# Performance work log

Hardware: AMD Instinct MI355X
Metric: run time of the kernel (lower is better)

Reference implementation:

```python
import jax, jax.numpy as jnp
import numpy as np

BETA = 0.9
THR = 1.0
ALPHA = 2.0  # snntorch surrogate.atan default

@jax.custom_vjp
def atan_spike(x):
    return (x > 0).astype(x.dtype)

def _atan_fwd(x):
    return atan_spike(x), x

def _atan_bwd(x, g):
    # snntorch ATan surrogate: alpha/2 / (1 + (pi/2 * alpha * x)^2)
    return (g * (ALPHA / 2.0) / (1.0 + (jnp.pi / 2.0 * ALPHA * x) ** 2),)

atan_spike.defvjp(_atan_fwd, _atan_bwd)

def setup_inputs() -> dict:
    key = jax.random.key(0)
    k = jax.random.split(key, 5)
    B, T, C, H, W = 128, 25, 3, 64, 64
    F, HID, O = C * H * W, 2048, 2
    bound1 = 1.0 / np.sqrt(F)
    boundo = 1.0 / np.sqrt(HID)
    return {
        "x": jax.random.normal(k[0], (B, T, C, H, W), jnp.float32),
        "W1": jax.random.uniform(k[1], (HID, F), jnp.float32, -bound1, bound1),
        "b1": jax.random.uniform(k[2], (HID,), jnp.float32, -bound1, bound1),
        "Wo": jax.random.uniform(k[3], (O, HID), jnp.float32, -boundo, boundo),
        "bo": jax.random.uniform(k[4], (O,), jnp.float32, -boundo, boundo),
    }

def reference(x, W1, b1, Wo, bo):
    B, T = x.shape[0], x.shape[1]
    HID, O = W1.shape[0], Wo.shape[0]
    xf = x.reshape(B, T, -1).transpose(1, 0, 2)  # [T, B, F]
    # fc1 for all timesteps at once (input is fixed per step)
    h_all = jnp.einsum('tbf,hf->tbh', xf, W1) + b1  # [T, B, HID]

    def step(carry, h):
        mem1, memo = carry
        # snntorch Leaky (reset_mechanism='subtract'): reset from previous mem
        r1 = atan_spike(mem1 - THR)
        mem1 = BETA * mem1 + h - r1 * THR
        s1 = atan_spike(mem1 - THR)
        o = s1 @ Wo.T + bo
        ro = atan_spike(memo - THR)
        memo = BETA * memo + o - ro * THR
        so = atan_spike(memo - THR)
        return (mem1, memo), so

    init = (jnp.zeros((B, HID), x.dtype), jnp.zeros((B, O), x.dtype))
    (_, _), spk_rec = jax.lax.scan(step, init, h_all)
    # train=False path: sum of output spikes over time
    return spk_rec.sum(axis=0)  # [B, O]
```

## Files before the change

kernel.cpp:

```cpp
#include <hip/hip_runtime.h>


#define T_STEPS 25
#define B_SZ    128
#define F_SZ    12288
#define HID_SZ  2048
#define KT      384
#define M_PAD   3328
#define UPB     156
#define PART_STRIDE ((size_t)M_PAD * HID_SZ)

typedef __attribute__((ext_vector_type(8))) _Float16 f16x8;
typedef __attribute__((ext_vector_type(4))) float f32x4;
typedef __attribute__((ext_vector_type(16))) float f32x16;

__device__ __forceinline__ void g2l16(const void* g, void* l) {
  __builtin_amdgcn_global_load_lds(
      (const __attribute__((address_space(1))) void*)g,
      (__attribute__((address_space(3))) void*)l, 16, 0, 0);
}

__device__ __forceinline__ void split8(f32x4 v0, f32x4 v1, f16x8& hi, f16x8& lo) {
#pragma unroll
  for (int j = 0; j < 4; ++j) {
    _Float16 h = (_Float16)v0[j];
    hi[j] = h;
    lo[j] = (_Float16)(v0[j] - (float)h);
    _Float16 h2 = (_Float16)v1[j];
    hi[4 + j] = h2;
    lo[4 + j] = (_Float16)(v1[j] - (float)h2);
  }
}

__global__ __launch_bounds__(256) void conv_w_kernel(
    const float* __restrict__ W1, char* __restrict__ B2) {
  const int total = 8 * KT * 256 * 4;
  for (int i = blockIdx.x * 256 + threadIdx.x; i < total; i += gridDim.x * 256) {
    const int s = i & 3;
    const int r = (i >> 2) & 255;
    const int rest = i >> 10;
    const int ks = rest % KT;
    const int nt = rest / KT;
    const float* src = W1 + ((size_t)(nt * 256 + r)) * F_SZ + ks * 32 + s * 8;
    float4 v0 = *(const float4*)src;
    float4 v1 = *(const float4*)(src + 4);
    float vf[8] = {v0.x, v0.y, v0.z, v0.w, v1.x, v1.y, v1.z, v1.w};
    f16x8 hi, lo;
#pragma unroll
    for (int j = 0; j < 8; ++j) {
      float vs = vf[j] * 128.0f;
      _Float16 h = (_Float16)vs;
      hi[j] = h;
      lo[j] = (_Float16)(vs - (float)h);
    }
    char* chunk = B2 + (size_t)rest * 32768;
    *(f16x8*)(chunk + s * 4096 + r * 16) = hi;
    *(f16x8*)(chunk + (s + 4) * 4096 + r * 16) = lo;
  }
}

__global__ __launch_bounds__(512, 1) void gemm_persist_kernel(
    const float* __restrict__ x, const char* __restrict__ B2,
    float* __restrict__ parts) {
  __shared__ __align__(16) char lds[131072];
  const int tid = threadIdx.x;
  const int l = tid & 63;
  const int w = tid >> 6;
  const int wm = w >> 2;
  const int wn = w & 3;
  const int lhalf = l >> 5;

  const int swz = ((blockIdx.x & 7) << 5) + (blockIdx.x >> 3);

  const int arow = (wm * 128 + (l & 31)) * 16;
  const int brow = (wn * 64 + (l & 31)) * 16;

  int u = swz * UPB;
  const int u1 = u + UPB;

  while (u < u1) {
    const int mnt = u / 384;
    const int kt0 = u - mnt * 384;
    const int rem_t = 384 - kt0, rem_u = u1 - u;
    const int seg = rem_t < rem_u ? rem_t : rem_u;
    const int ktN = kt0 + seg;
    const int nt = mnt / 13;
    const int mt = mnt - nt * 13;

    int m = mt * 256 + (tid & 255);
    if (m > 3199) m = 3199;
    const char* aRow = (const char*)(x +
        ((size_t)((m & 127) * T_STEPS + (m >> 7))) * F_SZ) + ((tid >> 8) << 4);
    const char* bBase = B2 + (size_t)nt * KT * 32768 + tid * 16;

#define STAGE(ktx)                                                        \
    do {                                                                  \
      char* d_ = (char*)lds + ((ktx) & 1) * 65536 + tid * 16;             \
      const char* as_ = aRow + (ktx) * 128;                               \
      const char* bs_ = bBase + (size_t)(ktx) * 32768;                    \
      g2l16(as_, d_);              g2l16(as_ + 32, d_ + 8192);            \
      g2l16(as_ + 64, d_ + 16384); g2l16(as_ + 96, d_ + 24576);           \
      g2l16(bs_, d_ + 32768);          g2l16(bs_ + 8192, d_ + 40960);     \
      g2l16(bs_ + 16384, d_ + 49152);  g2l16(bs_ + 24576, d_ + 57344);    \
    } while (0)

    f32x16 acc[4][2];
#pragma unroll
    for (int i = 0; i < 4; ++i)
#pragma unroll
      for (int j = 0; j < 2; ++j)
#pragma unroll
        for (int r = 0; r < 16; ++r) acc[i][j][r] = 0.f;

    STAGE(kt0);

    for (int kt = kt0; kt < ktN; ++kt) {
      __syncthreads();
      if (kt + 1 < ktN) STAGE(kt + 1);

      const char* la = (const char*)lds + (kt & 1) * 65536;
      const char* lb = la + 32768;

#pragma unroll
      for (int ks = 0; ks < 2; ++ks) {
        const int g = ks * 2 + lhalf;
        const int aBase = g * 8192 + arow;
        f16x8 ah[4], al[4];
#pragma unroll
        for (int mf = 0; mf < 4; ++mf) {
          f32x4 v0 = *(const f32x4*)(la + aBase + mf * 512);
          f32x4 v1 = *(const f32x4*)(la + aBase + 4096 + mf * 512);
          split8(v0, v1, ah[mf], al[mf]);
        }
#pragma unroll
        for (int nf = 0; nf < 2; ++nf) {
          f16x8 bh = *(const f16x8*)(lb + g * 4096 + brow + nf * 512);
          f16x8 bl = *(const f16x8*)(lb + 16384 + g * 4096 + brow + nf * 512);
          __builtin_amdgcn_s_setprio(1);
#pragma unroll
          for (int mf = 0; mf < 4; ++mf) {
            acc[mf][nf] = __builtin_amdgcn_mfma_f32_32x32x16_f16(ah[mf], bh, acc[mf][nf], 0, 0, 0);
            acc[mf][nf] = __builtin_amdgcn_mfma_f32_32x32x16_f16(ah[mf], bl, acc[mf][nf], 0, 0, 0);
            acc[mf][nf] = __builtin_amdgcn_mfma_f32_32x32x16_f16(al[mf], bh, acc[mf][nf], 0, 0, 0);
          }
          __builtin_amdgcn_s_setprio(0);
        }
      }
    }

    const int slot = swz - (mnt * 384) / UPB;
    float* dst = parts + (size_t)slot * PART_STRIDE;
    const int row0 = mt * 256 + wm * 128 + (lhalf << 2);
    const int col0 = nt * 256 + wn * 64 + (l & 31);
#pragma unroll
    for (int nf = 0; nf < 2; ++nf)
#pragma unroll
      for (int mf = 0; mf < 4; ++mf)
#pragma unroll
        for (int r = 0; r < 16; ++r) {
          const int row = row0 + mf * 32 + (r & 3) + ((r >> 2) << 3);
          dst[(size_t)row * HID_SZ + col0 + nf * 32] = acc[mf][nf][r];
        }
    u += seg;
    __syncthreads();
#undef STAGE
  }
}

__global__ __launch_bounds__(256) void gemm_h_kernel(
    const float* __restrict__ x, const float* __restrict__ W1,
    const float* __restrict__ b1, float* __restrict__ h_all) {
  __shared__ float As[16][128];
  __shared__ float Bs[16][128];
  const int tid = threadIdx.x;
  const int tx = tid & 15;
  const int ty = tid >> 4;
  const int m0 = blockIdx.x * 128;
  const int n0 = blockIdx.y * 128;
  const int lrow = tid >> 1;
  const int lcol = (tid & 1) * 8;
  const int gm = m0 + lrow;
  const int bb = gm & (B_SZ - 1);
  const int tt = gm >> 7;
  const float* aptr = x + ((size_t)bb * T_STEPS + tt) * F_SZ + lcol;
  const float* bptr = W1 + (size_t)(n0 + lrow) * F_SZ + lcol;
  float acc[8][8];
#pragma unroll
  for (int i = 0; i < 8; ++i)
#pragma unroll
    for (int j = 0; j < 8; ++j) acc[i][j] = 0.f;
  for (int k0 = 0; k0 < F_SZ; k0 += 16) {
    float4 av0 = *(const float4*)(aptr + k0);
    float4 av1 = *(const float4*)(aptr + k0 + 4);
    float4 bv0 = *(const float4*)(bptr + k0);
    float4 bv1 = *(const float4*)(bptr + k0 + 4);
    As[lcol + 0][lrow] = av0.x; As[lcol + 1][lrow] = av0.y;
    As[lcol + 2][lrow] = av0.z; As[lcol + 3][lrow] = av0.w;
    As[lcol + 4][lrow] = av1.x; As[lcol + 5][lrow] = av1.y;
    As[lcol + 6][lrow] = av1.z; As[lcol + 7][lrow] = av1.w;
    Bs[lcol + 0][lrow] = bv0.x; Bs[lcol + 1][lrow] = bv0.y;
    Bs[lcol + 2][lrow] = bv0.z; Bs[lcol + 3][lrow] = bv0.w;
    Bs[lcol + 4][lrow] = bv1.x; Bs[lcol + 5][lrow] = bv1.y;
    Bs[lcol + 6][lrow] = bv1.z; Bs[lcol + 7][lrow] = bv1.w;
    __syncthreads();
#pragma unroll
    for (int k = 0; k < 16; ++k) {
      float4 a0 = *(const float4*)&As[k][ty * 8];
      float4 a1 = *(const float4*)&As[k][ty * 8 + 4];
      float4 q0 = *(const float4*)&Bs[k][tx * 8];
      float4 q1 = *(const float4*)&Bs[k][tx * 8 + 4];
      float ar[8] = {a0.x, a0.y, a0.z, a0.w, a1.x, a1.y, a1.z, a1.w};
      float br[8] = {q0.x, q0.y, q0.z, q0.w, q1.x, q1.y, q1.z, q1.w};
#pragma unroll
      for (int i = 0; i < 8; ++i)
#pragma unroll
        for (int j = 0; j < 8; ++j)
          acc[i][j] = fmaf(ar[i], br[j], acc[i][j]);
    }
    __syncthreads();
  }
#pragma unroll
  for (int i = 0; i < 8; ++i) {
    const int gm2 = m0 + ty * 8 + i;
    float* orow = h_all + (size_t)gm2 * HID_SZ + n0 + tx * 8;
    const float* brow = b1 + n0 + tx * 8;
#pragma unroll
    for (int j = 0; j < 8; ++j) orow[j] = acc[i][j] + brow[j];
  }
}

__global__ __launch_bounds__(256) void lif_hidden_kernel(
    const float* __restrict__ parts, const float* __restrict__ b1,
    const float* __restrict__ Wo, float* __restrict__ oc, int mode) {
  const int b = blockIdx.x & 127;
  const int half = blockIdx.x >> 7;
  const int tid = threadIdx.x;
  const int h0 = half * 1024;
  float mem1[4], wo0[4], wo1[4], bv[4];
#pragma unroll
  for (int i = 0; i < 4; ++i) {
    const int hid = h0 + 256 * i + tid;
    mem1[i] = 0.f;
    wo0[i] = Wo[hid];
    wo1[i] = Wo[HID_SZ + hid];
    bv[i] = b1[hid];
  }
  __shared__ float partial[4][2];
  for (int t = 0; t < T_STEPS; ++t) {
    const int row = t * B_SZ + b;
    const size_t rowb = (size_t)row * HID_SZ;
    const int mt = row >> 8;
    float pr0 = 0.f, pr1 = 0.f;
#pragma unroll
    for (int i = 0; i < 4; ++i) {
      const int hid = h0 + 256 * i + tid;
      const size_t idx = rowb + hid;
      float h;
      if (mode == 2) {
        float s = parts[idx] + parts[idx + PART_STRIDE] +
                  parts[idx + 2 * PART_STRIDE];
        const int mnt = (hid >> 8) * 13 + mt;
        const int k0 = mnt * 384;
        if ((k0 + 383) / UPB - k0 / UPB + 1 == 4)
          s += parts[idx + 3 * PART_STRIDE];
        h = s * 0.0078125f + bv[i];
      } else {
        h = parts[idx];
      }
      float r1 = mem1[i] > 1.0f ? 1.0f : 0.0f;
      float m = 0.9f * mem1[i] + h - r1;
      mem1[i] = m;
      if (m > 1.0f) { pr0 += wo0[i]; pr1 += wo1[i]; }
    }
#pragma unroll
    for (int off = 32; off > 0; off >>= 1) {
      pr0 += __shfl_down(pr0, off);
      pr1 += __shfl_down(pr1, off);
    }
    if ((tid & 63) == 0) { partial[tid >> 6][0] = pr0; partial[tid >> 6][1] = pr1; }
    __syncthreads();
    if (tid == 0) {
      const size_t o = (((size_t)b * 2 + half) * T_STEPS + t) * 2;
      oc[o + 0] = partial[0][0] + partial[1][0] + partial[2][0] + partial[3][0];
      oc[o + 1] = partial[0][1] + partial[1][1] + partial[2][1] + partial[3][1];
    }
    __syncthreads();
  }
}

__global__ __launch_bounds__(128) void lif_out_kernel(
    const float* __restrict__ oc, const float* __restrict__ bo,
    float* __restrict__ out) {
  const int b = threadIdx.x;
  float memo0 = 0.f, memo1 = 0.f, a0 = 0.f, a1 = 0.f;
  const float bo0 = bo[0], bo1 = bo[1];
  for (int t = 0; t < T_STEPS; ++t) {
    const size_t i0 = (((size_t)b * 2 + 0) * T_STEPS + t) * 2;
    const size_t i1 = (((size_t)b * 2 + 1) * T_STEPS + t) * 2;
    float o0 = oc[i0] + oc[i1] + bo0;
    float o1 = oc[i0 + 1] + oc[i1 + 1] + bo1;
    float ro0 = memo0 > 1.0f ? 1.0f : 0.0f;
    float ro1 = memo1 > 1.0f ? 1.0f : 0.0f;
    memo0 = 0.9f * memo0 + o0 - ro0;
    memo1 = 0.9f * memo1 + o1 - ro1;
    a0 += memo0 > 1.0f ? 1.0f : 0.0f;
    a1 += memo1 > 1.0f ? 1.0f : 0.0f;
  }
  out[b * 2 + 0] = a0;
  out[b * 2 + 1] = a1;
}

extern "C" void kernel_launch(void* const* d_in, const int* in_sizes, int n_in,
                              void* d_out, int out_size, void* d_ws, size_t ws_size,
                              hipStream_t stream) {
  const float* x  = (const float*)d_in[0];
  const float* W1 = (const float*)d_in[1];
  const float* b1 = (const float*)d_in[2];
  const float* Wo = (const float*)d_in[3];
  const float* bo = (const float*)d_in[4];
  float* out = (float*)d_out;

  const size_t part_bytes = PART_STRIDE * 4;
  const size_t b2_bytes = (size_t)8 * KT * 32768;
  const size_t oc_bytes = (size_t)128 * 2 * T_STEPS * 2 * 4;
  char* ws = (char*)d_ws;
  float* parts = (float*)ws;

  if (ws_size >= 4 * part_bytes + b2_bytes + oc_bytes) {
    char* B2 = ws + 4 * part_bytes;
    float* oc = (float*)(B2 + b2_bytes);
    conv_w_kernel<<<2048, 256, 0, stream>>>(W1, B2);
    gemm_persist_kernel<<<256, 512, 0, stream>>>(x, B2, parts);
    lif_hidden_kernel<<<256, 256, 0, stream>>>(parts, b1, Wo, oc, 2);
    lif_out_kernel<<<1, 128, 0, stream>>>(oc, bo, out);
  } else {
    float* oc = (float*)(ws + part_bytes);
    dim3 grid(25, 16);
    gemm_h_kernel<<<grid, 256, 0, stream>>>(x, W1, b1, parts);
    lif_hidden_kernel<<<256, 256, 0, stream>>>(parts, b1, Wo, oc, 0);
    lif_out_kernel<<<1, 128, 0, stream>>>(oc, bo, out);
  }
}
```

Baseline: 672.1 us.

## Replace persistent stream-K GEMM with fixed split-K tiles and triple-buffered A staging

Replaces the persistent stream-K scheduler, in which 256 blocks walked a linear unit range, with a grid of 416 blocks. Each block owns one 256x256 tile and a fixed quarter of K (split-K by 4). The A operand now uses three LDS buffers staged two steps ahead, B uses two buffers, and explicit vmcnt waits with raw barriers replace __syncthreads. The LIF kernel sums all four partials unconditionally. This removes the segment bookkeeping and aims at deeper load/compute overlap, at the cost of more LDS per block and losing the balanced work distribution across CUs.

```diff
diff --git a/kernel.cpp b/kernel.cpp
--- a/kernel.cpp
+++ b/kernel.cpp
@@ -7,7 +7,6 @@
 #define HID_SZ  2048
 #define KT      384
 #define M_PAD   3328
-#define UPB     156
 #define PART_STRIDE ((size_t)M_PAD * HID_SZ)
 
 typedef __attribute__((ext_vector_type(8))) _Float16 f16x8;
@@ -59,10 +58,10 @@
   }
 }
 
-__global__ __launch_bounds__(512, 1) void gemm_persist_kernel(
+__global__ __launch_bounds__(512, 1) void gemm_tile_kernel(
     const float* __restrict__ x, const char* __restrict__ B2,
     float* __restrict__ parts) {
-  __shared__ __align__(16) char lds[131072];
+  __shared__ __align__(16) char lds[163840];
   const int tid = threadIdx.x;
   const int l = tid & 63;
   const int w = tid >> 6;
@@ -70,101 +69,113 @@
   const int wn = w & 3;
   const int lhalf = l >> 5;
 
-  const int swz = ((blockIdx.x & 7) << 5) + (blockIdx.x >> 3);
+  const int bid = blockIdx.x;
+  const int mt = bid >> 5;
+  const int nt = (bid >> 2) & 7;
+  const int ksp = bid & 3;
+  const int kt0 = ksp * 96;
+  const int ktN = kt0 + 96;
 
   const int arow = (wm * 128 + (l & 31)) * 16;
   const int brow = (wn * 64 + (l & 31)) * 16;
 
-  int u = swz * UPB;
-  const int u1 = u + UPB;
-
-  while (u < u1) {
-    const int mnt = u / 384;
-    const int kt0 = u - mnt * 384;
-    const int rem_t = 384 - kt0, rem_u = u1 - u;
-    const int seg = rem_t < rem_u ? rem_t : rem_u;
-    const int ktN = kt0 + seg;
-    const int nt = mnt / 13;
-    const int mt = mnt - nt * 13;
-
-    int m = mt * 256 + (tid & 255);
-    if (m > 3199) m = 3199;
-    const char* aRow = (const char*)(x +
-        ((size_t)((m & 127) * T_STEPS + (m >> 7))) * F_SZ) + ((tid >> 8) << 4);
-    const char* bBase = B2 + (size_t)nt * KT * 32768 + tid * 16;
-
-#define STAGE(ktx)                                                        \
-    do {                                                                  \
-      char* d_ = (char*)lds + ((ktx) & 1) * 65536 + tid * 16;             \
-      const char* as_ = aRow + (ktx) * 128;                               \
-      const char* bs_ = bBase + (size_t)(ktx) * 32768;                    \
-      g2l16(as_, d_);              g2l16(as_ + 32, d_ + 8192);            \
-      g2l16(as_ + 64, d_ + 16384); g2l16(as_ + 96, d_ + 24576);           \
-      g2l16(bs_, d_ + 32768);          g2l16(bs_ + 8192, d_ + 40960);     \
-      g2l16(bs_ + 16384, d_ + 49152);  g2l16(bs_ + 24576, d_ + 57344);    \
-    } while (0)
-
-    f32x16 acc[4][2];
-#pragma unroll
-    for (int i = 0; i < 4; ++i)
-#pragma unroll
-      for (int j = 0; j < 2; ++j)
-#pragma unroll
-        for (int r = 0; r < 16; ++r) acc[i][j][r] = 0.f;
-
-    STAGE(kt0);
-
-    for (int kt = kt0; kt < ktN; ++kt) {
-      __syncthreads();
-      if (kt + 1 < ktN) STAGE(kt + 1);
-
-      const char* la = (const char*)lds + (kt & 1) * 65536;
-      const char* lb = la + 32768;
-
-#pragma unroll
-      for (int ks = 0; ks < 2; ++ks) {
-        const int g = ks * 2 + lhalf;
-        const int aBase = g * 8192 + arow;
-        f16x8 ah[4], al[4];
+  int m = mt * 256 + (tid & 255);
+  if (m > 3199) m = 3199;
+  const char* aRow = (const char*)(x +
+      ((size_t)((m & 127) * T_STEPS + (m >> 7))) * F_SZ) + ((tid >> 8) << 4);
+  const char* bBase = B2 + (size_t)nt * KT * 32768 + tid * 16;
+
+#define STAGE_A(ktx, buf)                                                \
+  do {                                                                   \
+    char* d_ = (char*)lds + (buf) * 32768 + tid * 16;                    \
+    const char* s_ = aRow + (ktx) * 128;                                 \
+    g2l16(s_, d_);              g2l16(s_ + 32, d_ + 8192);               \
+    g2l16(s_ + 64, d_ + 16384); g2l16(s_ + 96, d_ + 24576);              \
+  } while (0)
+#define STAGE_B(ktx, buf)                                                \
+  do {                                                                   \
+    char* d_ = (char*)lds + 98304 + (buf) * 32768 + tid * 16;            \
+    const char* s_ = bBase + (size_t)(ktx) * 32768;                      \
+    g2l16(s_, d_);                  g2l16(s_ + 8192, d_ + 8192);         \
+    g2l16(s_ + 16384, d_ + 16384);  g2l16(s_ + 24576, d_ + 24576);       \
+  } while (0)
+
+  f32x16 acc[4][2];
+#pragma unroll
+  for (int i = 0; i < 4; ++i)
+#pragma unroll
+    for (int j = 0; j < 2; ++j)
+#pragma unroll
+      for (int r = 0; r < 16; ++r) acc[i][j][r] = 0.f;
+
+  STAGE_A(kt0, 0);
+  STAGE_B(kt0, 0);
+  STAGE_A(kt0 + 1, 1);
+
+  int ab = 0;
+  int ab2 = 2;
+  int bb = 0;
+
+  for (int kt = kt0; kt < ktN; ++kt) {
+    if (kt + 1 < ktN) {
+      asm volatile("s_waitcnt vmcnt(4)" ::: "memory");
+    } else {
+      asm volatile("s_waitcnt vmcnt(0)" ::: "memory");
+    }
+    __builtin_amdgcn_s_barrier();
+    __builtin_amdgcn_sched_barrier(0);
+
+    if (kt + 1 < ktN) STAGE_B(kt + 1, bb ^ 1);
+    if (kt + 2 < ktN) STAGE_A(kt + 2, ab2);
+
+    const char* la = (const char*)lds + ab * 32768;
+    const char* lb = (const char*)lds + 98304 + bb * 32768;
+
+#pragma unroll
+    for (int ks = 0; ks < 2; ++ks) {
+      const int g = ks * 2 + lhalf;
+      const int aBase = g * 8192 + arow;
+      f16x8 ah[4], al[4];
+#pragma unroll
+      for (int mf = 0; mf < 4; ++mf) {
+        f32x4 v0 = *(const f32x4*)(la + aBase + mf * 512);
+        f32x4 v1 = *(const f32x4*)(la + aBase + 4096 + mf * 512);
+        split8(v0, v1, ah[mf], al[mf]);
+      }
+#pragma unroll
+      for (int nf = 0; nf < 2; ++nf) {
+        f16x8 bh = *(const f16x8*)(lb + g * 4096 + brow + nf * 512);
+        f16x8 bl = *(const f16x8*)(lb + 16384 + g * 4096 + brow + nf * 512);
+        __builtin_amdgcn_s_setprio(1);
 #pragma unroll
         for (int mf = 0; mf < 4; ++mf) {
-          f32x4 v0 = *(const f32x4*)(la + aBase + mf * 512);
-          f32x4 v1 = *(const f32x4*)(la + aBase + 4096 + mf * 512);
-          split8(v0, v1, ah[mf], al[mf]);
+          acc[mf][nf] = __builtin_amdgcn_mfma_f32_32x32x16_f16(ah[mf], bh, acc[mf][nf], 0, 0, 0);
+          acc[mf][nf] = __builtin_amdgcn_mfma_f32_32x32x16_f16(ah[mf], bl, acc[mf][nf], 0, 0, 0);
+          acc[mf][nf] = __builtin_amdgcn_mfma_f32_32x32x16_f16(al[mf], bh, acc[mf][nf], 0, 0, 0);
         }
-#pragma unroll
-        for (int nf = 0; nf < 2; ++nf) {
-          f16x8 bh = *(const f16x8*)(lb + g * 4096 + brow + nf * 512);
-          f16x8 bl = *(const f16x8*)(lb + 16384 + g * 4096 + brow + nf * 512);
-          __builtin_amdgcn_s_setprio(1);
-#pragma unroll
-          for (int mf = 0; mf < 4; ++mf) {
-            acc[mf][nf] = __builtin_amdgcn_mfma_f32_32x32x16_f16(ah[mf], bh, acc[mf][nf], 0, 0, 0);
-            acc[mf][nf] = __builtin_amdgcn_mfma_f32_32x32x16_f16(ah[mf], bl, acc[mf][nf], 0, 0, 0);
-            acc[mf][nf] = __builtin_amdgcn_mfma_f32_32x32x16_f16(al[mf], bh, acc[mf][nf], 0, 0, 0);
-          }
-          __builtin_amdgcn_s_setprio(0);
-        }
+        __builtin_amdgcn_s_setprio(0);
       }
     }
 
-    const int slot = swz - (mnt * 384) / UPB;
-    float* dst = parts + (size_t)slot * PART_STRIDE;
-    const int row0 = mt * 256 + wm * 128 + (lhalf << 2);
-    const int col0 = nt * 256 + wn * 64 + (l & 31);
-#pragma unroll
-    for (int nf = 0; nf < 2; ++nf)
-#pragma unroll
-      for (int mf = 0; mf < 4; ++mf)
-#pragma unroll
-        for (int r = 0; r < 16; ++r) {
-          const int row = row0 + mf * 32 + (r & 3) + ((r >> 2) << 3);
-          dst[(size_t)row * HID_SZ + col0 + nf * 32] = acc[mf][nf][r];
-        }
-    u += seg;
-    __syncthreads();
-#undef STAGE
-  }
+    ab = (ab == 2) ? 0 : ab + 1;
+    ab2 = (ab2 == 2) ? 0 : ab2 + 1;
+    bb ^= 1;
+  }
+
+  float* dst = parts + (size_t)ksp * PART_STRIDE;
+  const int row0 = mt * 256 + wm * 128 + (lhalf << 2);
+  const int col0 = nt * 256 + wn * 64 + (l & 31);
+#pragma unroll
+  for (int nf = 0; nf < 2; ++nf)
+#pragma unroll
+    for (int mf = 0; mf < 4; ++mf)
+#pragma unroll
+      for (int r = 0; r < 16; ++r) {
+        const int row = row0 + mf * 32 + (r & 3) + ((r >> 2) << 3);
+        dst[(size_t)row * HID_SZ + col0 + nf * 32] = acc[mf][nf][r];
+      }
+#undef STAGE_A
+#undef STAGE_B
 }
 
 __global__ __launch_bounds__(256) void gemm_h_kernel(
@@ -249,20 +260,15 @@
   for (int t = 0; t < T_STEPS; ++t) {
     const int row = t * B_SZ + b;
     const size_t rowb = (size_t)row * HID_SZ;
-    const int mt = row >> 8;
     float pr0 = 0.f, pr1 = 0.f;
 #pragma unroll
     for (int i = 0; i < 4; ++i) {
       const int hid = h0 + 256 * i + tid;
       const size_t idx = rowb + hid;
       float h;
-      if (mode == 2) {
-        float s = parts[idx] + parts[idx + PART_STRIDE] +
-                  parts[idx + 2 * PART_STRIDE];
-        const int mnt = (hid >> 8) * 13 + mt;
-        const int k0 = mnt * 384;
-        if ((k0 + 383) / UPB - k0 / UPB + 1 == 4)
-          s += parts[idx + 3 * PART_STRIDE];
+      if (mode == 1) {
+        float s = (parts[idx] + parts[idx + PART_STRIDE]) +
+                  (parts[idx + 2 * PART_STRIDE] + parts[idx + 3 * PART_STRIDE]);
         h = s * 0.0078125f + bv[i];
       } else {
         h = parts[idx];
@@ -330,14 +336,14 @@
     char* B2 = ws + 4 * part_bytes;
     float* oc = (float*)(B2 + b2_bytes);
     conv_w_kernel<<<2048, 256, 0, stream>>>(W1, B2);
-    gemm_persist_kernel<<<256, 512, 0, stream>>>(x, B2, parts);
-    lif_hidden_kernel<<<256, 256, 0, stream>>>(parts, b1, Wo, oc, 2);
+    gemm_tile_kernel<<<416, 512, 0, stream>>>(x, B2, parts);
+    lif_hidden_kernel<<<256, 256, 0, stream>>>(parts, b1, Wo, oc, 1);
     lif_out_kernel<<<1, 128, 0, stream>>>(oc, bo, out);
   } else {
     float* oc = (float*)(ws + part_bytes);
     dim3 grid(25, 16);
-    gemm_h_kernel<<<grid, 256, 0, stream>>>(x, W1, b1, parts);
-    lif_hidden_kernel<<<256, 256, 0, stream>>>(parts, b1, Wo, oc, 0);
+    gemm_h_kernel<<<grid, 256, 0, stream>>>(x, W1, b1, (float*)ws);
+    lif_hidden_kernel<<<256, 256, 0, stream>>>((const float*)ws, b1, Wo, oc, 0);
     lif_out_kernel<<<1, 128, 0, stream>>>(oc, bo, out);
   }
 }
```

After: 676.3 us. No clear change (+0.6%).
